# Kernel optimization log

Measured on AMD Instinct MI355X. Metric: run time of the kernel, lower is better.

Reference implementation:

```python
import jax, jax.numpy as jnp
import numpy as np

B, N, F_IN, H = 16, 2048, 6, 64
NEG_INF = -jnp.inf


def setup_inputs() -> dict:
    key = jax.random.key(0)
    ks = jax.random.split(key, 16)
    x = jax.random.normal(ks[0], (B, N, F_IN), dtype=jnp.float32)
    adj = jax.random.bernoulli(ks[1], 0.5, (B, N, N)).astype(jnp.int32)
    valid = int(N * 0.9)
    mask = jnp.broadcast_to((jnp.arange(N) < valid).astype(jnp.float32)[None, :, None], (B, N, 1))
    mask = jnp.array(mask)

    def lin(k, fi, fo):
        return jax.random.normal(k, (fi, fo), dtype=jnp.float32) / np.sqrt(fi)

    return {
        'x': x, 'adj': adj, 'mask': mask,
        'W1': lin(ks[2], F_IN, H), 'a_src1': lin(ks[3], H, 1), 'a_dst1': lin(ks[4], H, 1),
        'W2': lin(ks[5], H, H), 'a_src2': lin(ks[6], H, 1), 'a_dst2': lin(ks[7], H, 1),
        'actor_w1': lin(ks[8], H, 32), 'actor_b1': jnp.zeros((32,), jnp.float32),
        'actor_w2': lin(ks[9], 32, 1), 'actor_b2': jnp.zeros((1,), jnp.float32),
        'critic_w1': lin(ks[10], H, 32), 'critic_b1': jnp.zeros((32,), jnp.float32),
        'critic_w2': lin(ks[11], 32, 1), 'critic_b2': jnp.zeros((1,), jnp.float32),
    }


def gat_layer(x, adj, mask, W, a_src, a_dst):
    h = x @ W                                    # [B,N,H]
    s = h @ a_src                                # [B,N,1]
    d = h @ a_dst                                # [B,N,1]
    e = jax.nn.leaky_relu(s + jnp.swapaxes(d, -1, -2), 0.2)   # [B,N,N]
    e = jnp.where(adj == 0, NEG_INF, e)
    e = jnp.where(jnp.swapaxes(mask, -1, -2) == 0, NEG_INF, e)
    alpha = jnp.nan_to_num(jax.nn.softmax(e, axis=-1))
    out = alpha @ h + h
    return jax.nn.elu(out) * mask


def reference(x, adj, mask, W1, a_src1, a_dst1, W2, a_src2, a_dst2,
              actor_w1, actor_b1, actor_w2, actor_b2,
              critic_w1, critic_b1, critic_w2, critic_b2):
    h = gat_layer(x, adj, mask, W1, a_src1, a_dst1)
    h = gat_layer(h, adj, mask, W2, a_src2, a_dst2)
    logits = (jax.nn.elu(h @ actor_w1 + actor_b1) @ actor_w2 + actor_b2)[..., 0]  # [B,N]
    sum_h = h.sum(axis=1)                                   # [B,H]
    valid_counts = jnp.clip(mask.sum(axis=1), 1.0)          # [B,1]
    global_h = sum_h / valid_counts
    value = (jax.nn.elu(global_h @ critic_w1 + critic_b1) @ critic_w2 + critic_b2)[..., 0]  # [B]
    return logits, value
```

## Files before the change

### kernel.cpp

```cpp
#include <hip/hip_runtime.h>
#include <hip/hip_bf16.h>

constexpr int kB = 16;
constexpr int kN = 2048;
constexpr int kH = 64;
constexpr int kF = 6;

typedef short s16x8 __attribute__((ext_vector_type(8)));
typedef float f32x4 __attribute__((ext_vector_type(4)));

__device__ __forceinline__ unsigned short f2bf(float f) {
  __hip_bfloat16 h = __float2bfloat16(f);
  unsigned short u;
  __builtin_memcpy(&u, &h, 2);
  return u;
}

__device__ __forceinline__ float bf2f(unsigned short u) {
  unsigned int b = ((unsigned int)u) << 16;
  float f;
  __builtin_memcpy(&f, &b, 4);
  return f;
}

__device__ __forceinline__ float eluf(float x) {
  return x > 0.0f ? x : __expf(x) - 1.0f;
}

__device__ __forceinline__ unsigned int pack8(uint4 a, uint4 b) {
  unsigned int t1 = (a.y << 1) + a.x;
  unsigned int t2 = (a.w << 1) + a.z;
  unsigned int n0 = (t2 << 2) + t1;
  unsigned int u1 = (b.y << 1) + b.x;
  unsigned int u2 = (b.w << 1) + b.z;
  unsigned int n1 = (u2 << 2) + u1;
  return (n1 << 4) + n0;
}

__global__ __launch_bounds__(256) void k_embed(
    const float* __restrict__ x, const float* __restrict__ W,
    const float* __restrict__ asrc, const float* __restrict__ adst,
    const float* __restrict__ mask,
    float* __restrict__ hf, unsigned short* __restrict__ hT,
    unsigned int* __restrict__ uvpk, float* __restrict__ Rr,
    float* __restrict__ sumh,
    const float* __restrict__ W2,
    unsigned short* __restrict__ w2thi, unsigned short* __restrict__ w2tlo) {
  __shared__ float lh[64][65];
  __shared__ float psd[2][4][64];
  const int r0 = blockIdx.x * 64;
  const int b = r0 >> 11;
  const int i0 = r0 & (kN - 1);
  const int t = threadIdx.x;
  const int k = t & 63;
  const int w = t >> 6;
  if (blockIdx.x == 0) {
#pragma unroll
    for (int i = 0; i < 4; ++i) sumh[t + 256 * i] = 0.0f;
  }
  if (blockIdx.x == 1) {
#pragma unroll
    for (int i = 0; i < 16; ++i) {
      const int idx = t + 256 * i;
      const int col = idx & 63, kk = idx >> 6;
      const float wv = W2[kk * kH + col];
      const unsigned short hh = f2bf(wv);
      w2thi[col * 64 + kk] = hh;
      w2tlo[col * 64 + kk] = f2bf(wv - bf2f(hh));
    }
  }
  for (int it = 0; it < 16; ++it) {
    const int rl = w * 16 + it;
    const int row = r0 + rl;
    float h = 0.0f;
#pragma unroll
    for (int f = 0; f < kF; ++f) h = fmaf(x[(size_t)row * kF + f], W[f * kH + k], h);
    lh[rl][k] = h;
    hf[(size_t)row * kH + k] = h;
  }
  __syncthreads();
  float sp = 0.0f, dp = 0.0f;
#pragma unroll
  for (int kk = 0; kk < 16; ++kk) {
    const int k2 = w * 16 + kk;
    const float hv = lh[k][k2];
    sp = fmaf(hv, asrc[k2], sp);
    dp = fmaf(hv, adst[k2], dp);
  }
  psd[0][w][k] = sp;
  psd[1][w][k] = dp;
  __syncthreads();
  if (t < 64) {
    const float s = psd[0][0][t] + psd[0][1][t] + psd[0][2][t] + psd[0][3][t];
    const float d = psd[1][0][t] + psd[1][1][t] + psd[1][2][t] + psd[1][3][t];
    const int row = r0 + t;
    const bool mv = mask[row] != 0.0f;
    const float u = mv ? __expf(d) : 0.0f;
    const float v = mv ? __expf(0.2f * d) : 0.0f;
    uvpk[row] = ((unsigned int)f2bf(u) << 16) | f2bf(v);
    Rr[row] = __expf(-0.8f * s);
  }
  const size_t tb = (size_t)b * kN * kH + (size_t)(i0 >> 5) * 2048;
  for (int it = 0; it < 16; ++it) {
    const int kk = w * 16 + it;
    hT[tb + (size_t)(k >> 5) * 2048 + kk * 32 + (k & 31)] = f2bf(lh[k][kk]);
  }
}

template <bool PACK, bool TAIL, bool EMB>
__global__ __launch_bounds__(256) void k_attn(
    const int* __restrict__ adj, unsigned int* __restrict__ bits,
    const unsigned short* __restrict__ hT,
    const unsigned int* __restrict__ uvpk, const float* __restrict__ Rr,
    const float* __restrict__ hres, const float* __restrict__ mask,
    const float* __restrict__ aw1, const float* __restrict__ ab1,
    const float* __restrict__ aw2, const float* __restrict__ ab2,
    float* __restrict__ logits, float* __restrict__ sumh,
    const unsigned short* __restrict__ w2thi, const unsigned short* __restrict__ w2tlo,
    const float* __restrict__ asrc2, const float* __restrict__ adst2,
    float* __restrict__ h2res, unsigned short* __restrict__ hT2,
    unsigned int* __restrict__ uv2, float* __restrict__ Rr2) {
  __shared__ __align__(16) char smem[32896];
  unsigned int* uvl = (unsigned int*)smem;
  unsigned int* blw = (unsigned int*)(smem + 8192);
  unsigned short* hbase = (unsigned short*)(smem + 16512);
  int* mxp = (int*)&blw[64];
  int* rfp = (int*)&blw[129];

  const int bid0 = blockIdx.x;
  const int swz = (bid0 & 7) * 128 + (bid0 >> 3);
  const int b = swz >> 6;
  const int rb = swz & 63;
  const int row0 = rb * 32;

  const int t = threadIdx.x;
  const int wv = t >> 6;
  const int l = t & 63;
  const int r = l & 15;
  const int g = l >> 4;
  const int rt = wv & 1;
  const int hf2 = wv >> 1;
  const int rloc = rt * 16 + r;

  if (t == 0) { *mxp = -1; *rfp = 0; }

  {
    const uint4* src = (const uint4*)(uvpk + (size_t)b * kN);
    ((uint4*)uvl)[t] = src[t];
    ((uint4*)uvl)[t + 256] = src[t + 256];
  }

  const unsigned short* hTb = hT + (size_t)b * kN * kH;
  {
    *(uint4*)(hbase + 0 * 2048 + t * 8) = *(const uint4*)(hTb + t * 8);
    *(uint4*)(hbase + 1 * 2048 + t * 8) = *(const uint4*)(hTb + (size_t)1 * 2048 + t * 8);
  }
  uint4 hc0 = *(const uint4*)(hTb + (size_t)2 * 2048 + t * 8);
  uint4 hc1 = *(const uint4*)(hTb + (size_t)3 * 2048 + t * 8);
  uint4 hn0 = {}, hn1 = {};

  const int brow = t >> 3;
  const int bc = t & 7;
  const int bh = bc >> 2;
  const int bq4 = bc & 3;
  const int* adjLp = adj + ((size_t)b * kN + row0 + brow) * kN + bh * 32 + bq4 * 8;
  uint4 qcA = {}, qcB = {}, qnA = {}, qnB = {};
  if (PACK) {
    const uint4 a0 = *(const uint4*)(adjLp);
    const uint4 a1 = *(const uint4*)(adjLp + 4);
    ((unsigned char*)blw)[(brow * 65 + bh) * 4 + bq4] = (unsigned char)pack8(a0, a1);
    qcA = *(const uint4*)(adjLp + 64);
    qcB = *(const uint4*)(adjLp + 68);
  } else {
#pragma unroll
    for (int ii = 0; ii < 8; ++ii) {
      const int idx = ii * 256 + t;
      const int rr2 = idx >> 6, wj = idx & 63;
      blw[rr2 * 65 + wj] = bits[((size_t)b * kN + row0 + rr2) * 64 + wj];
    }
  }

  const float Ri = Rr[(size_t)b * kN + row0 + rloc];
  __syncthreads();

  {
    int lm = -1;
#pragma unroll
    for (int i = 0; i < 8; ++i)
      if (uvl[t * 8 + i] != 0u) lm = t * 8 + i;
    if (lm >= 0) atomicMax(mxp, lm);
    if (t < 32 && mask[(size_t)b * kN + row0 + t] != 0.0f) atomicOr(rfp, 1);
  }
  __syncthreads();
  const int mxv = *mxp;
  const int ntj = (mxv < 0) ? 0 : ((mxv >> 6) + 1);
  const bool ract = (*rfp != 0);

  f32x4 acc0 = {0.f, 0.f, 0.f, 0.f}, acc1 = {0.f, 0.f, 0.f, 0.f};
  f32x4 acc2 = {0.f, 0.f, 0.f, 0.f}, acc3 = {0.f, 0.f, 0.f, 0.f};
  f32x4 accz = {0.f, 0.f, 0.f, 0.f};
  s16x8 ones;
#pragma unroll
  for (int e = 0; e < 8; ++e) ones[e] = (r == 0) ? (short)0x3F80 : (short)0;

  if (ract) {
    for (int jt = 0; jt < ntj; ++jt) {
      if (jt < ntj - 2) {
        hn0 = *(const uint4*)(hTb + (size_t)(2 * jt + 4) * 2048 + t * 8);
        hn1 = *(const uint4*)(hTb + (size_t)(2 * jt + 5) * 2048 + t * 8);
        if (PACK) {
          qnA = *(const uint4*)(adjLp + (size_t)(jt + 2) * 64);
          qnB = *(const uint4*)(adjLp + (size_t)(jt + 2) * 64 + 4);
        }
      }
      if (jt < ntj - 1) {
        const int buf = (jt + 1) & 1;
        *(uint4*)(hbase + (buf * 2 + 0) * 2048 + t * 8) = hc0;
        *(uint4*)(hbase + (buf * 2 + 1) * 2048 + t * 8) = hc1;
        if (PACK)
          ((unsigned char*)blw)[(brow * 65 + 2 * jt + 2 + bh) * 4 + bq4] =
              (unsigned char)pack8(qcA, qcB);
      }

      const unsigned int bw = blw[rloc * 65 + 2 * jt + hf2];
      const unsigned int byt = (bw >> (g * 8)) & 0xffu;
      const unsigned int* uvp = uvl + (2 * jt + hf2) * 32 + g * 8;
      const uint4 ua = *(const uint4*)uvp;
      const uint4 ub = *(const uint4*)(uvp + 4);
      union { s16x8 v; unsigned int w[4]; } afu;
      {
        const unsigned int uvw[8] = {ua.x, ua.y, ua.z, ua.w, ub.x, ub.y, ub.z, ub.w};
#pragma unroll
        for (int p = 0; p < 4; ++p) {
          unsigned int ulb = uvw[2 * p] & 0xFFFF0000u, vlb = uvw[2 * p] << 16;
          unsigned int uhb = uvw[2 * p + 1] & 0xFFFF0000u, vhb = uvw[2 * p + 1] << 16;
          float ulf, vlf, uhf, vhf;
          __builtin_memcpy(&ulf, &ulb, 4); __builtin_memcpy(&vlf, &vlb, 4);
          __builtin_memcpy(&uhf, &uhb, 4); __builtin_memcpy(&vhf, &vhb, 4);
          const float vall = fmaxf(ulf, Ri * vlf);
          const float valh = fmaxf(uhf, Ri * vhf);
          unsigned int lbits, hbits;
          __builtin_memcpy(&lbits, &vall, 4); __builtin_memcpy(&hbits, &valh, 4);
          lbits = (byt & (1u << (2 * p))) ? lbits : 0u;
          hbits = (byt & (1u << (2 * p + 1))) ? hbits : 0u;
          afu.w[p] = (hbits & 0xFFFF0000u) | (lbits >> 16);
        }
      }
      const unsigned short* cur = hbase + ((jt & 1) * 2 + hf2) * 2048 + r * 32 + g * 8;
      const s16x8 f0 = *(const s16x8*)(cur);
      const s16x8 f1 = *(const s16x8*)(cur + 512);
      const s16x8 f2 = *(const s16x8*)(cur + 1024);
      const s16x8 f3 = *(const s16x8*)(cur + 1536);

      acc0 = __builtin_amdgcn_mfma_f32_16x16x32_bf16(afu.v, f0, acc0, 0, 0, 0);
      acc1 = __builtin_amdgcn_mfma_f32_16x16x32_bf16(afu.v, f1, acc1, 0, 0, 0);
      acc2 = __builtin_amdgcn_mfma_f32_16x16x32_bf16(afu.v, f2, acc2, 0, 0, 0);
      acc3 = __builtin_amdgcn_mfma_f32_16x16x32_bf16(afu.v, f3, acc3, 0, 0, 0);
      accz = __builtin_amdgcn_mfma_f32_16x16x32_bf16(afu.v, ones, accz, 0, 0, 0);

      asm volatile("s_waitcnt lgkmcnt(0)" ::: "memory");
      __builtin_amdgcn_s_barrier();
      hc0 = hn0; hc1 = hn1;
      if (PACK) { qcA = qnA; qcB = qnB; }
    }
  }

  float* psumF = (float*)(smem + 16512);
  float* zsumF = (float*)(smem + 16512 + 8448);
  if (hf2 == 1) {
#pragma unroll
    for (int q = 0; q < 4; ++q) {
      const int lrow = rt * 16 + g * 4 + q;
      psumF[lrow * 66 + r + 0]  = acc0[q];
      psumF[lrow * 66 + r + 16] = acc1[q];
      psumF[lrow * 66 + r + 32] = acc2[q];
      psumF[lrow * 66 + r + 48] = acc3[q];
      if (r == 0) zsumF[lrow] = accz[q];
    }
  }
  if (PACK) {
#pragma unroll
    for (int ii = 0; ii < 8; ++ii) {
      const int idx = ii * 256 + t;
      const int rr2 = idx >> 6, wj = idx & 63;
      bits[((size_t)b * kN + row0 + rr2) * 64 + wj] = blw[rr2 * 65 + wj];
    }
  }
  __syncthreads();
  float* lhFF = (float*)smem;
  if (hf2 == 0) {
#pragma unroll
    for (int q = 0; q < 4; ++q) {
      const int lrow = rt * 16 + g * 4 + q;
      const float zq = __shfl(accz[q], (l & 48)) + zsumF[lrow];
      const float inv = (zq > 0.0f) ? 1.0f / zq : 0.0f;
      const size_t rowg = (size_t)b * kN + row0 + lrow;
      const float mk = mask[rowg];
      const float* hrp = hres + rowg * kH;
      const float o0 = eluf(fmaf(acc0[q] + psumF[lrow * 66 + r + 0],  inv, hrp[r + 0]))  * mk;
      const float o1 = eluf(fmaf(acc1[q] + psumF[lrow * 66 + r + 16], inv, hrp[r + 16])) * mk;
      const float o2 = eluf(fmaf(acc2[q] + psumF[lrow * 66 + r + 32], inv, hrp[r + 32])) * mk;
      const float o3 = eluf(fmaf(acc3[q] + psumF[lrow * 66 + r + 48], inv, hrp[r + 48])) * mk;
      lhFF[lrow * 65 + r + 0]  = o0;
      lhFF[lrow * 65 + r + 16] = o1;
      lhFF[lrow * 65 + r + 32] = o2;
      lhFF[lrow * 65 + r + 48] = o3;
    }
  }

  if (EMB) {
    __syncthreads();
    const int ntb = hf2 * 2;
    s16x8 ah[2], al[2];
    {
      const float* arow = lhFF + (rt * 16 + r) * 65;
#pragma unroll
      for (int ks = 0; ks < 2; ++ks) {
#pragma unroll
        for (int j = 0; j < 8; ++j) {
          const float v = arow[ks * 32 + g * 8 + j];
          const unsigned short hh = f2bf(v);
          ah[ks][j] = (short)hh;
          al[ks][j] = (short)f2bf(v - bf2f(hh));
        }
      }
    }
    f32x4 e0 = {0.f, 0.f, 0.f, 0.f}, e1 = {0.f, 0.f, 0.f, 0.f};
#pragma unroll
    for (int ks = 0; ks < 2; ++ks) {
      const int kof = ks * 32 + g * 8;
      {
        const s16x8 bhi = *(const s16x8*)(w2thi + (ntb * 16 + r) * 64 + kof);
        const s16x8 blo = *(const s16x8*)(w2tlo + (ntb * 16 + r) * 64 + kof);
        e0 = __builtin_amdgcn_mfma_f32_16x16x32_bf16(ah[ks], bhi, e0, 0, 0, 0);
        e0 = __builtin_amdgcn_mfma_f32_16x16x32_bf16(al[ks], bhi, e0, 0, 0, 0);
        e0 = __builtin_amdgcn_mfma_f32_16x16x32_bf16(ah[ks], blo, e0, 0, 0, 0);
      }
      {
        const s16x8 bhi = *(const s16x8*)(w2thi + ((ntb + 1) * 16 + r) * 64 + kof);
        const s16x8 blo = *(const s16x8*)(w2tlo + ((ntb + 1) * 16 + r) * 64 + kof);
        e1 = __builtin_amdgcn_mfma_f32_16x16x32_bf16(ah[ks], bhi, e1, 0, 0, 0);
        e1 = __builtin_amdgcn_mfma_f32_16x16x32_bf16(al[ks], bhi, e1, 0, 0, 0);
        e1 = __builtin_amdgcn_mfma_f32_16x16x32_bf16(ah[ks], blo, e1, 0, 0, 0);
      }
    }
    float* lh2F = (float*)(smem + 16512);
#pragma unroll
    for (int q = 0; q < 4; ++q) {
      const int lrow = rt * 16 + g * 4 + q;
      lh2F[lrow * 66 + ntb * 16 + r] = e0[q];
      lh2F[lrow * 66 + (ntb + 1) * 16 + r] = e1[q];
      const size_t rowg = (size_t)b * kN + row0 + lrow;
      h2res[rowg * kH + ntb * 16 + r] = e0[q];
      h2res[rowg * kH + (ntb + 1) * 16 + r] = e1[q];
    }
    __syncthreads();
    {
      const int kr = t & 31, wc = t >> 5;
      const size_t tb2 = (size_t)b * kN * kH + (size_t)rb * 2048;
#pragma unroll
      for (int it = 0; it < 8; ++it) {
        const int c = wc * 8 + it;
        hT2[tb2 + c * 32 + kr] = f2bf(lh2F[kr * 66 + c]);
      }
    }
    {
      const int rw = t >> 3, c0 = (t & 7) * 8;
      float sp = 0.0f, dp = 0.0f;
#pragma unroll
      for (int j = 0; j < 8; ++j) {
        const float hv = lh2F[rw * 66 + c0 + j];
        sp = fmaf(hv, asrc2[c0 + j], sp);
        dp = fmaf(hv, adst2[c0 + j], dp);
      }
#pragma unroll
      for (int o = 4; o; o >>= 1) {
        sp += __shfl_xor(sp, o);
        dp += __shfl_xor(dp, o);
      }
      if ((t & 7) == 0) {
        const size_t rowg = (size_t)b * kN + row0 + rw;
        const bool mv = mask[rowg] != 0.0f;
        const float u = mv ? __expf(dp) : 0.0f;
        const float v = mv ? __expf(0.2f * dp) : 0.0f;
        uv2[rowg] = ((unsigned int)f2bf(u) << 16) | f2bf(v);
        Rr2[rowg] = __expf(-0.8f * sp);
      }
    }
  }

  if (TAIL) {
    __syncthreads();
    const int ln = t & 31;
    const int grp = t >> 5;
#pragma unroll
    for (int rr2 = 0; rr2 < 4; ++rr2) {
      const int lrow = grp * 4 + rr2;
      float accA = ab1[ln];
#pragma unroll 8
      for (int m = 0; m < kH; ++m) accA = fmaf(lhFF[lrow * 65 + m], aw1[m * 32 + ln], accA);
      float p = eluf(accA) * aw2[ln];
#pragma unroll
      for (int o = 16; o; o >>= 1) p += __shfl_xor(p, o, 32);
      if (ln == 0) logits[(size_t)b * kN + row0 + lrow] = p + ab2[0];
    }
    float cs = 0.0f;
    const int kcol = t & 63;
    const int seg = t >> 6;
#pragma unroll
    for (int ii = 0; ii < 8; ++ii) cs += lhFF[(seg * 8 + ii) * 65 + kcol];
    float* csF = (float*)(smem + 16512 + 8704);
    csF[seg * 64 + kcol] = cs;
    __syncthreads();
    if (t < 64) atomicAdd(&sumh[b * 64 + t], csF[t] + csF[64 + t] + csF[128 + t] + csF[192 + t]);
  }
}

__global__ __launch_bounds__(64) void k_critic2(
    const float* __restrict__ sumh, const float* __restrict__ mask,
    const float* __restrict__ cw1, const float* __restrict__ cb1,
    const float* __restrict__ cw2, const float* __restrict__ cb2,
    float* __restrict__ value) {
  __shared__ float lgh[64];
  const int b = blockIdx.x, t = threadIdx.x;
  float c = 0.0f;
#pragma unroll
  for (int ii = 0; ii < 32; ++ii) c += mask[(size_t)b * kN + t + 64 * ii];
#pragma unroll
  for (int off = 32; off; off >>= 1) c += __shfl_xor(c, off);
  lgh[t] = sumh[b * 64 + t] / fmaxf(c, 1.0f);
  __syncthreads();
  if (t < 32) {
    float acc = cb1[t];
#pragma unroll 8
    for (int m = 0; m < kH; ++m) acc = fmaf(lgh[m], cw1[m * 32 + t], acc);
    float p = eluf(acc) * cw2[t];
#pragma unroll
    for (int off = 16; off; off >>= 1) p += __shfl_xor(p, off, 32);
    if (t == 0) value[b] = p + cb2[0];
  }
}

extern "C" void kernel_launch(void* const* d_in, const int* in_sizes, int n_in,
                              void* d_out, int out_size, void* d_ws, size_t ws_size,
                              hipStream_t stream) {
  const float* x = (const float*)d_in[0];
  const int* adj = (const int*)d_in[1];
  const float* mask = (const float*)d_in[2];
  const float* W1 = (const float*)d_in[3];
  const float* asrc1 = (const float*)d_in[4];
  const float* adst1 = (const float*)d_in[5];
  const float* W2 = (const float*)d_in[6];
  const float* asrc2 = (const float*)d_in[7];
  const float* adst2 = (const float*)d_in[8];
  const float* aw1 = (const float*)d_in[9];
  const float* ab1 = (const float*)d_in[10];
  const float* aw2 = (const float*)d_in[11];
  const float* ab2 = (const float*)d_in[12];
  const float* cw1 = (const float*)d_in[13];
  const float* cb1 = (const float*)d_in[14];
  const float* cw2 = (const float*)d_in[15];
  const float* cb2 = (const float*)d_in[16];
  float* logits = (float*)d_out;
  float* value = (float*)d_out + kB * kN;

  char* ws = (char*)d_ws;
  size_t off = 0;
  auto take = [&](size_t bytes) {
    char* p = ws + off;
    off = (off + bytes + 255) & ~(size_t)255;
    return p;
  };
  unsigned int* bits = (unsigned int*)take((size_t)kB * kN * (kN / 8));
  float* hA = (float*)take((size_t)kB * kN * kH * 4);
  float* hA2 = (float*)take((size_t)kB * kN * kH * 4);
  unsigned short* hT1 = (unsigned short*)take((size_t)kB * kN * kH * 2);
  unsigned short* hT2 = (unsigned short*)take((size_t)kB * kN * kH * 2);
  unsigned int* uv1 = (unsigned int*)take((size_t)kB * kN * 4);
  unsigned int* uv2 = (unsigned int*)take((size_t)kB * kN * 4);
  float* R1 = (float*)take((size_t)kB * kN * 4);
  float* R2 = (float*)take((size_t)kB * kN * 4);
  float* sumh = (float*)take(kB * kH * 4);
  unsigned short* w2thi = (unsigned short*)take(64 * 64 * 2);
  unsigned short* w2tlo = (unsigned short*)take(64 * 64 * 2);

  k_embed<<<kB * kN / 64, 256, 0, stream>>>(x, W1, asrc1, adst1, mask, hA, hT1, uv1, R1,
                                            sumh, W2, w2thi, w2tlo);
  k_attn<true, false, true><<<kB * 64, 256, 0, stream>>>(
      adj, bits, hT1, uv1, R1, hA, mask, aw1, ab1, aw2, ab2, logits, sumh,
      w2thi, w2tlo, asrc2, adst2, hA2, hT2, uv2, R2);
  k_attn<false, true, false><<<kB * 64, 256, 0, stream>>>(
      adj, bits, hT2, uv2, R2, hA2, mask, aw1, ab1, aw2, ab2, logits, sumh,
      nullptr, nullptr, nullptr, nullptr, nullptr, nullptr, nullptr, nullptr);
  k_critic2<<<kB, 64, 0, stream>>>(sumh, mask, cw1, cb1, cw2, cb2, value);
}
```

Baseline: 113.4 us.

## Double attention row tile to 64 rows with 512-thread blocks

Each attention block now handles 64 destination rows with 8 waves instead of 32 rows with 4 waves, halving the grid to 512 blocks. The staged hT column tile in shared memory is reused across twice as many rows, which halves redundant hT/uv global reads per row. Shared memory grows to about 44KB per block and the per-thread streaming loads shrink, at the cost of fewer blocks and possibly lower occupancy. Several partially visible indexing paths (blw sizing, psum layout, tail reductions) had to be adapted and may be fragile.

```diff
diff --git a/kernel.cpp b/kernel.cpp
--- a/kernel.cpp
+++ b/kernel.cpp
@@ -108,7 +108,7 @@
 }
 
 template <bool PACK, bool TAIL, bool EMB>
-__global__ __launch_bounds__(256) void k_attn(
+__global__ __launch_bounds__(512) void k_attn(
     const int* __restrict__ adj, unsigned int* __restrict__ bits,
     const unsigned short* __restrict__ hT,
     const unsigned int* __restrict__ uvpk, const float* __restrict__ Rr,
@@ -120,26 +120,27 @@
     const float* __restrict__ asrc2, const float* __restrict__ adst2,
     float* __restrict__ h2res, unsigned short* __restrict__ hT2,
     unsigned int* __restrict__ uv2, float* __restrict__ Rr2) {
-  __shared__ __align__(16) char smem[32896];
+  __shared__ __align__(16) char smem[44032];
   unsigned int* uvl = (unsigned int*)smem;
   unsigned int* blw = (unsigned int*)(smem + 8192);
-  unsigned short* hbase = (unsigned short*)(smem + 16512);
+  unsigned short* hbase = (unsigned short*)(smem + 24832);
+  char* hbc = (char*)hbase;
   int* mxp = (int*)&blw[64];
   int* rfp = (int*)&blw[129];
 
   const int bid0 = blockIdx.x;
-  const int swz = (bid0 & 7) * 128 + (bid0 >> 3);
-  const int b = swz >> 6;
-  const int rb = swz & 63;
-  const int row0 = rb * 32;
+  const int swz = (bid0 & 7) * 64 + (bid0 >> 3);
+  const int b = swz >> 5;
+  const int rb = swz & 31;
+  const int row0 = rb * 64;
 
   const int t = threadIdx.x;
   const int wv = t >> 6;
   const int l = t & 63;
   const int r = l & 15;
   const int g = l >> 4;
-  const int rt = wv & 1;
-  const int hf2 = wv >> 1;
+  const int hf2 = wv & 1;
+  const int rt = wv >> 1;
   const int rloc = rt * 16 + r;
 
   if (t == 0) { *mxp = -1; *rfp = 0; }
@@ -147,17 +148,13 @@
   {
     const uint4* src = (const uint4*)(uvpk + (size_t)b * kN);
     ((uint4*)uvl)[t] = src[t];
-    ((uint4*)uvl)[t + 256] = src[t + 256];
   }
 
   const unsigned short* hTb = hT + (size_t)b * kN * kH;
-  {
-    *(uint4*)(hbase + 0 * 2048 + t * 8) = *(const uint4*)(hTb + t * 8);
-    *(uint4*)(hbase + 1 * 2048 + t * 8) = *(const uint4*)(hTb + (size_t)1 * 2048 + t * 8);
-  }
-  uint4 hc0 = *(const uint4*)(hTb + (size_t)2 * 2048 + t * 8);
-  uint4 hc1 = *(const uint4*)(hTb + (size_t)3 * 2048 + t * 8);
-  uint4 hn0 = {}, hn1 = {};
+  const char* hTc = (const char*)hTb;
+  *(uint4*)(hbc + t * 16) = *(const uint4*)(hTc + t * 16);
+  uint4 hc0 = *(const uint4*)(hTc + 8192 + t * 16);
+  uint4 hn0 = {};
 
   const int brow = t >> 3;
   const int bc = t & 7;
@@ -174,7 +171,7 @@
   } else {
 #pragma unroll
     for (int ii = 0; ii < 8; ++ii) {
-      const int idx = ii * 256 + t;
+      const int idx = ii * 512 + t;
       const int rr2 = idx >> 6, wj = idx & 63;
       blw[rr2 * 65 + wj] = bits[((size_t)b * kN + row0 + rr2) * 64 + wj];
     }
@@ -186,10 +183,10 @@
   {
     int lm = -1;
 #pragma unroll
-    for (int i = 0; i < 8; ++i)
-      if (uvl[t * 8 + i] != 0u) lm = t * 8 + i;
+    for (int i = 0; i < 4; ++i)
+      if (uvl[t * 4 + i] != 0u) lm = t * 4 + i;
     if (lm >= 0) atomicMax(mxp, lm);
-    if (t < 32 && mask[(size_t)b * kN + row0 + t] != 0.0f) atomicOr(rfp, 1);
+    if (t < 64 && mask[(size_t)b * kN + row0 + t] != 0.0f) atomicOr(rfp, 1);
   }
   __syncthreads();
   const int mxv = *mxp;
@@ -206,17 +203,14 @@
   if (ract) {
     for (int jt = 0; jt < ntj; ++jt) {
       if (jt < ntj - 2) {
-        hn0 = *(const uint4*)(hTb + (size_t)(2 * jt + 4) * 2048 + t * 8);
-        hn1 = *(const uint4*)(hTb + (size_t)(2 * jt + 5) * 2048 + t * 8);
+        hn0 = *(const uint4*)(hTc + (size_t)(jt + 2) * 8192 + t * 16);
         if (PACK) {
           qnA = *(const uint4*)(adjLp + (size_t)(jt + 2) * 64);
           qnB = *(const uint4*)(adjLp + (size_t)(jt + 2) * 64 + 4);
         }
       }
       if (jt < ntj - 1) {
-        const int buf = (jt + 1) & 1;
-        *(uint4*)(hbase + (buf * 2 + 0) * 2048 + t * 8) = hc0;
-        *(uint4*)(hbase + (buf * 2 + 1) * 2048 + t * 8) = hc1;
+        *(uint4*)(hbc + ((jt + 1) & 1) * 8192 + t * 16) = hc0;
         if (PACK)
           ((unsigned char*)blw)[(brow * 65 + 2 * jt + 2 + bh) * 4 + bq4] =
               (unsigned char)pack8(qcA, qcB);
@@ -260,13 +254,13 @@
 
       asm volatile("s_waitcnt lgkmcnt(0)" ::: "memory");
       __builtin_amdgcn_s_barrier();
-      hc0 = hn0; hc1 = hn1;
+      hc0 = hn0;
       if (PACK) { qcA = qnA; qcB = qnB; }
     }
   }
 
-  float* psumF = (float*)(smem + 16512);
-  float* zsumF = (float*)(smem + 16512 + 8448);
+  float* psumF = (float*)(smem + 24832);
+  float* zsumF = (float*)(smem + 41728);
   if (hf2 == 1) {
 #pragma unroll
     for (int q = 0; q < 4; ++q) {
@@ -281,7 +275,7 @@
   if (PACK) {
 #pragma unroll
     for (int ii = 0; ii < 8; ++ii) {
-      const int idx = ii * 256 + t;
+      const int idx = ii * 512 + t;
       const int rr2 = idx >> 6, wj = idx & 63;
       bits[((size_t)b * kN + row0 + rr2) * 64 + wj] = blw[rr2 * 65 + wj];
     }
@@ -344,7 +338,7 @@
         e1 = __builtin_amdgcn_mfma_f32_16x16x32_bf16(ah[ks], blo, e1, 0, 0, 0);
       }
     }
-    float* lh2F = (float*)(smem + 16512);
+    float* lh2F = (float*)(smem + 24832);
 #pragma unroll
     for (int q = 0; q < 4; ++q) {
       const int lrow = rt * 16 + g * 4 + q;
@@ -356,12 +350,14 @@
     }
     __syncthreads();
     {
-      const int kr = t & 31, wc = t >> 5;
-      const size_t tb2 = (size_t)b * kN * kH + (size_t)rb * 2048;
+      const int ch = t >> 8;
+      const int tt = t & 255;
+      const int kr = tt & 31, wc = tt >> 5;
+      const size_t tb2 = (size_t)b * kN * kH + (size_t)(rb * 2 + ch) * 2048;
 #pragma unroll
       for (int it = 0; it < 8; ++it) {
         const int c = wc * 8 + it;
-        hT2[tb2 + c * 32 + kr] = f2bf(lh2F[kr * 66 + c]);
+        hT2[tb2 + c * 32 + kr] = f2bf(lh2F[(ch * 32 + kr) * 66 + c]);
       }
     }
     {
@@ -409,10 +405,15 @@
     const int seg = t >> 6;
 #pragma unroll
     for (int ii = 0; ii < 8; ++ii) cs += lhFF[(seg * 8 + ii) * 65 + kcol];
-    float* csF = (float*)(smem + 16512 + 8704);
+    float* csF = (float*)(smem + 41984);
     csF[seg * 64 + kcol] = cs;
     __syncthreads();
-    if (t < 64) atomicAdd(&sumh[b * 64 + t], csF[t] + csF[64 + t] + csF[128 + t] + csF[192 + t]);
+    if (t < 64) {
+      float s = 0.0f;
+#pragma unroll
+      for (int k2 = 0; k2 < 8; ++k2) s += csF[k2 * 64 + t];
+      atomicAdd(&sumh[b * 64 + t], s);
+    }
   }
 }
 
@@ -486,10 +487,10 @@
 
   k_embed<<<kB * kN / 64, 256, 0, stream>>>(x, W1, asrc1, adst1, mask, hA, hT1, uv1, R1,
                                             sumh, W2, w2thi, w2tlo);
-  k_attn<true, false, true><<<kB * 64, 256, 0, stream>>>(
+  k_attn<true, false, true><<<kB * 32, 512, 0, stream>>>(
       adj, bits, hT1, uv1, R1, hA, mask, aw1, ab1, aw2, ab2, logits, sumh,
       w2thi, w2tlo, asrc2, adst2, hA2, hT2, uv2, R2);
-  k_attn<false, true, false><<<kB * 64, 256, 0, stream>>>(
+  k_attn<false, true, false><<<kB * 32, 512, 0, stream>>>(
       adj, bits, hT2, uv2, R2, hA2, mask, aw1, ab1, aw2, ab2, logits, sumh,
       nullptr, nullptr, nullptr, nullptr, nullptr, nullptr, nullptr, nullptr);
   k_critic2<<<kB, 64, 0, stream>>>(sumh, mask, cw1, cb1, cw2, cb2, value);
```

After: 110.5 us. 2.5% less time.
